# Kernel optimization log

Measured on AMD Instinct MI355X. Metric: run time of the kernel, lower is better.

Reference implementation:

```python
import jax, jax.numpy as jnp
import numpy as np

B, S, D = 8, 2048, 512

def setup_inputs() -> dict:
    key = jax.random.key(0)
    ks = jax.random.split(key, 9)
    scale = 1.0 / np.sqrt(D)
    q = jax.random.normal(ks[0], (B, S, D), dtype=jnp.float32)
    k = jax.random.normal(ks[1], (B, S, D), dtype=jnp.float32)
    v = jax.random.normal(ks[2], (B, S, D), dtype=jnp.float32)
    # causal mask, broadcast over batch: True = attend
    mask = jnp.tril(jnp.ones((S, S), dtype=bool))[None, :, :]
    Wq = jax.random.normal(ks[3], (D, D), dtype=jnp.float32) * scale
    bq = jax.random.normal(ks[4], (D,), dtype=jnp.float32) * scale
    Wk = jax.random.normal(ks[5], (D, D), dtype=jnp.float32) * scale
    bk = jax.random.normal(ks[6], (D,), dtype=jnp.float32) * scale
    Wv = jax.random.normal(ks[7], (D, D), dtype=jnp.float32) * scale
    bv = jax.random.normal(ks[8], (D,), dtype=jnp.float32) * scale
    return {"q": q, "k": k, "v": v, "mask": mask,
            "Wq": Wq, "bq": bq, "Wk": Wk, "bk": bk, "Wv": Wv, "bv": bv}

def reference(q, k, v, mask, Wq, bq, Wk, bk, Wv, bv):
    # torch nn.Linear: x @ W^T + b
    Q = jnp.einsum('bsd,ed->bse', q, Wq) + bq
    K = jnp.einsum('bsd,ed->bse', k, Wk) + bk
    V = jnp.einsum('bsd,ed->bse', v, Wv) + bv
    scores = jnp.einsum('bqd,bkd->bqk', Q, K) / jnp.sqrt(jnp.float32(D))
    scores = jnp.where(mask, scores, jnp.float32(-1e9))
    prob = jax.nn.softmax(scores, axis=-1)
    out = jnp.einsum('bqk,bkd->bqd', prob, V)
    return out
```

## Files before the change

### kernel.cpp

```cpp
#include <hip/hip_runtime.h>
#include <stdint.h>
#include <stddef.h>

typedef _Float16 half8 __attribute__((ext_vector_type(8)));
typedef float f32x4 __attribute__((ext_vector_type(4)));

#define SCALE_QK 0.04419417382415922f

__device__ __forceinline__ void gload16(const void* g, void* lds) {
  __builtin_amdgcn_global_load_lds(
      (const __attribute__((address_space(1))) void*)g,
      (__attribute__((address_space(3))) void*)lds,
      16, 0, 0);
}

template<bool A_F32>
__device__ __forceinline__ void run_kloop(const void* Arow0, const _Float16* Brow0,
                                          int lda, int ldb, int kIters,
                                          _Float16* As, _Float16* Bs,
                                          f32x4 (&acc)[4][4])
{
  const int tid  = threadIdx.x;
  const int lane = tid & 63;
  const int w    = tid >> 6;
  const int wm   = w >> 1, wn = w & 1;
  const int srow = tid >> 3;
  const int sg   = tid & 7;
  const int swz  = sg ^ (srow & 7);
  const int fr   = lane & 15;
  const int fq   = lane >> 4;
  const int fx   = lane & 7;

  for (int it = 0; it < kIters; ++it) {
    const int k0 = it * 64;
    __syncthreads();
    if constexpr (A_F32) {
      const float* A = (const float*)Arow0;
      #pragma unroll
      for (int i = 0; i < 4; ++i) {
        const float* src = A + (size_t)(i*32 + srow) * lda + (k0 + sg*8);
        f32x4 x = *(const f32x4*)src;
        f32x4 y = *(const f32x4*)(src + 4);
        half8 h;
        h[0]=(_Float16)x[0]; h[1]=(_Float16)x[1]; h[2]=(_Float16)x[2]; h[3]=(_Float16)x[3];
        h[4]=(_Float16)y[0]; h[5]=(_Float16)y[1]; h[6]=(_Float16)y[2]; h[7]=(_Float16)y[3];
        *(half8*)(As + (i*32 + srow)*64 + swz*8) = h;
      }
    } else {
      const _Float16* A = (const _Float16*)Arow0;
      #pragma unroll
      for (int i = 0; i < 4; ++i) {
        const _Float16* src = A + (size_t)(i*32 + srow) * lda + (k0 + swz*8);
        gload16(src, As + i*2048 + w*512);
      }
    }
    #pragma unroll
    for (int i = 0; i < 4; ++i) {
      const _Float16* src = Brow0 + (size_t)(i*32 + srow) * ldb + (k0 + swz*8);
      gload16(src, Bs + i*2048 + w*512);
    }
    __syncthreads();

    #pragma unroll
    for (int ks = 0; ks < 2; ++ks) {
      half8 av[4], bv[4];
      const int slot = (ks*4 + fq) ^ fx;
      #pragma unroll
      for (int i = 0; i < 4; ++i) {
        av[i] = *(const half8*)(As + (wm*64 + i*16 + fr)*64 + slot*8);
        bv[i] = *(const half8*)(Bs + (wn*64 + i*16 + fr)*64 + slot*8);
      }
      #pragma unroll
      for (int i = 0; i < 4; ++i) {
        #pragma unroll
        for (int j = 0; j < 4; ++j) {
          acc[i][j] = __builtin_amdgcn_mfma_f32_16x16x32_f16(av[i], bv[j], acc[i][j], 0, 0, 0);
        }
      }
    }
  }
}

__global__ __launch_bounds__(256) void k_cvtw(const float* __restrict__ Wq,
                                              const float* __restrict__ Wk,
                                              const float* __restrict__ Wv,
                                              _Float16* __restrict__ Wb)
{
  const int t = blockIdx.x * 256 + threadIdx.x;
  const int base = t * 8;
  const int z = base >> 18;
  const int off = base & 262143;
  const float* src = (z == 0) ? Wq : ((z == 1) ? Wk : Wv);
  f32x4 a = *(const f32x4*)(src + off);
  f32x4 b = *(const f32x4*)(src + off + 4);
  half8 h;
  h[0]=(_Float16)a[0]; h[1]=(_Float16)a[1]; h[2]=(_Float16)a[2]; h[3]=(_Float16)a[3];
  h[4]=(_Float16)b[0]; h[5]=(_Float16)b[1]; h[6]=(_Float16)b[2]; h[7]=(_Float16)b[3];
  *(half8*)(Wb + base) = h;
}

__global__ __launch_bounds__(256) void k_proj(const float* __restrict__ q,
                                              const float* __restrict__ k,
                                              const float* __restrict__ v,
                                              const _Float16* __restrict__ Wb,
                                              const float* __restrict__ bq,
                                              const float* __restrict__ bk,
                                              const float* __restrict__ bv,
                                              _Float16* __restrict__ Qb,
                                              _Float16* __restrict__ Kb,
                                              _Float16* __restrict__ Vb)
{
  __shared__ __align__(16) _Float16 As[128*64];
  __shared__ __align__(16) _Float16 Bs[128*64];
  const int z = blockIdx.z;
  const float* A     = (z == 0) ? q  : (z == 1) ? k  : v;
  const float* bia   = (z == 0) ? bq : (z == 1) ? bk : bv;
  const _Float16* B  = Wb + (size_t)z * 512 * 512;
  _Float16* C        = (z == 0) ? Qb : (z == 1) ? Kb : Vb;
  const int mt = blockIdx.y, nt = blockIdx.x;

  f32x4 acc[4][4] = {};
  run_kloop<true>(A + (size_t)mt*128*512, B + (size_t)nt*128*512, 512, 512, 8, As, Bs, acc);

  const int lane = threadIdx.x & 63, w = threadIdx.x >> 6;
  const int wm = w >> 1, wn = w & 1;
  const int fr = lane & 15, fq = lane >> 4;
  #pragma unroll
  for (int j = 0; j < 4; ++j) {
    const int col = nt*128 + wn*64 + j*16 + fr;
    const float bval = bia[col];
    #pragma unroll
    for (int i = 0; i < 4; ++i) {
      const int row = mt*128 + wm*64 + i*16 + fq*4;
      #pragma unroll
      for (int r = 0; r < 4; ++r)
        C[(size_t)(row + r) * 512 + col] = (_Float16)(acc[i][j][r] + bval);
    }
  }
}

__global__ __launch_bounds__(256) void k_trans(const _Float16* __restrict__ Vb,
                                               _Float16* __restrict__ Vt)
{
  __shared__ __align__(16) _Float16 t[64][72];
  const int st = blockIdx.x, dt = blockIdx.y, b = blockIdx.z;
  const int r = threadIdx.x >> 2, g = threadIdx.x & 3;
  const _Float16* src = Vb + ((size_t)b*2048 + st*64 + r)*512 + dt*64 + g*16;
  half8 v0 = *(const half8*)src;
  half8 v1 = *(const half8*)(src + 8);
  *(half8*)&t[r][g*16]     = v0;
  *(half8*)&t[r][g*16 + 8] = v1;
  __syncthreads();
  half8 o0, o1;
  #pragma unroll
  for (int i2 = 0; i2 < 8; ++i2) o0[i2] = t[g*16 + i2][r];
  #pragma unroll
  for (int i2 = 0; i2 < 8; ++i2) o1[i2] = t[g*16 + 8 + i2][r];
  _Float16* dst = Vt + ((size_t)b*512 + dt*64 + r)*2048 + st*64 + g*16;
  *(half8*)dst       = o0;
  *(half8*)(dst + 8) = o1;
}

__global__ __launch_bounds__(256) void k_scores(const _Float16* __restrict__ Qb,
                                                const _Float16* __restrict__ Kb,
                                                _Float16* __restrict__ P)
{
  const int kt = blockIdx.x, qt = blockIdx.y, b = blockIdx.z;
  if (kt > qt) return;
  __shared__ __align__(16) _Float16 As[128*64];
  __shared__ __align__(16) _Float16 Bs[128*64];
  f32x4 acc[4][4] = {};
  run_kloop<false>(Qb + ((size_t)b*2048 + qt*128)*512,
                   Kb + ((size_t)b*2048 + kt*128)*512,
                   512, 512, 8, As, Bs, acc);
  const int lane = threadIdx.x & 63, w = threadIdx.x >> 6;
  const int wm = w >> 1, wn = w & 1;
  const int fr = lane & 15, fq = lane >> 4;
  #pragma unroll
  for (int i = 0; i < 4; ++i) {
    const int row = qt*128 + wm*64 + i*16 + fq*4;
    #pragma unroll
    for (int j = 0; j < 4; ++j) {
      const int col = kt*128 + wn*64 + j*16 + fr;
      #pragma unroll
      for (int r = 0; r < 4; ++r)
        P[((size_t)b*2048 + row + r) * 2048 + col] = (_Float16)(acc[i][j][r] * SCALE_QK);
    }
  }
}

__global__ __launch_bounds__(256) void k_softmax(_Float16* __restrict__ P)
{
  const int lane = threadIdx.x & 63;
  const int row  = blockIdx.x * 4 + (threadIdx.x >> 6);
  const int qIdx = row & 2047;
  _Float16* p = P + (size_t)row * 2048;
  const int L    = qIdx + 1;
  const int Lpad = ((qIdx >> 7) + 1) * 128;

  float m = -1e30f;
  for (int i0 = lane * 8; i0 < L; i0 += 512) {
    if (i0 + 8 <= L) {
      half8 x = *(const half8*)(p + i0);
      #pragma unroll
      for (int j2 = 0; j2 < 8; ++j2) m = fmaxf(m, (float)x[j2]);
    } else {
      for (int j2 = 0; i0 + j2 < L; ++j2) m = fmaxf(m, (float)p[i0 + j2]);
    }
  }
  #pragma unroll
  for (int s = 1; s < 64; s <<= 1) m = fmaxf(m, __shfl_xor(m, s, 64));

  float lsum = 0.f;
  for (int i0 = lane * 8; i0 < L; i0 += 512) {
    if (i0 + 8 <= L) {
      half8 x = *(const half8*)(p + i0);
      #pragma unroll
      for (int j2 = 0; j2 < 8; ++j2) lsum += __expf((float)x[j2] - m);
    } else {
      for (int j2 = 0; i0 + j2 < L; ++j2) lsum += __expf((float)p[i0 + j2] - m);
    }
  }
  #pragma unroll
  for (int s = 1; s < 64; s <<= 1) lsum += __shfl_xor(lsum, s, 64);
  const float inv = 1.0f / lsum;

  for (int i0 = lane * 8; i0 < Lpad; i0 += 512) {
    half8 o;
    if (i0 + 8 <= L) {
      half8 x = *(const half8*)(p + i0);
      #pragma unroll
      for (int j2 = 0; j2 < 8; ++j2) o[j2] = (_Float16)(__expf((float)x[j2] - m) * inv);
    } else {
      #pragma unroll
      for (int j2 = 0; j2 < 8; ++j2) {
        const int idx = i0 + j2;
        o[j2] = (idx < L) ? (_Float16)(__expf((float)p[idx] - m) * inv) : (_Float16)0.f;
      }
    }
    *(half8*)(p + i0) = o;
  }
}

__global__ __launch_bounds__(256) void k_pv(const _Float16* __restrict__ P,
                                            const _Float16* __restrict__ Vt,
                                            float* __restrict__ Out)
{
  const int dt = blockIdx.x, b = blockIdx.z;
  const int yr = blockIdx.y;
  const int qt = (yr & 1) ? (15 - (yr >> 1)) : (yr >> 1);
  __shared__ __align__(16) _Float16 As[128*64];
  __shared__ __align__(16) _Float16 Bs[128*64];
  f32x4 acc[4][4] = {};
  run_kloop<false>(P  + ((size_t)b*2048 + qt*128)*2048,
                   Vt + ((size_t)b*512  + dt*128)*2048,
                   2048, 2048, (qt + 1) * 2, As, Bs, acc);
  const int lane = threadIdx.x & 63, w = threadIdx.x >> 6;
  const int wm = w >> 1, wn = w & 1;
  const int fr = lane & 15, fq = lane >> 4;
  #pragma unroll
  for (int i = 0; i < 4; ++i) {
    const int row = qt*128 + wm*64 + i*16 + fq*4;
    #pragma unroll
    for (int j = 0; j < 4; ++j) {
      const int col = dt*128 + wn*64 + j*16 + fr;
      #pragma unroll
      for (int r = 0; r < 4; ++r)
        Out[((size_t)b*2048 + row + r) * 512 + col] = acc[i][j][r];
    }
  }
}

extern "C" void kernel_launch(void* const* d_in, const int* in_sizes, int n_in,
                              void* d_out, int out_size, void* d_ws, size_t ws_size,
                              hipStream_t stream) {
  (void)in_sizes; (void)n_in; (void)out_size;
  const float* q  = (const float*)d_in[0];
  const float* k  = (const float*)d_in[1];
  const float* v  = (const float*)d_in[2];
  const float* Wq = (const float*)d_in[4];
  const float* bq = (const float*)d_in[5];
  const float* Wk = (const float*)d_in[6];
  const float* bk = (const float*)d_in[7];
  const float* Wv = (const float*)d_in[8];
  const float* bv = (const float*)d_in[9];

  const size_t OFF_P  = 0;
  const size_t OFF_Q  = (size_t)64 << 20;
  const size_t OFF_K  = (size_t)80 << 20;
  const size_t OFF_V  = (size_t)96 << 20;
  const size_t OFF_VT = (size_t)112 << 20;
  const size_t OFF_W  = (size_t)128 << 20;
  const size_t NEEDED = OFF_W + (size_t)3 * 512 * 512 * sizeof(_Float16);
  if (ws_size < NEEDED) return;

  char* ws = (char*)d_ws;
  _Float16* P  = (_Float16*)(ws + OFF_P);
  _Float16* Qb = (_Float16*)(ws + OFF_Q);
  _Float16* Kb = (_Float16*)(ws + OFF_K);
  _Float16* Vb = (_Float16*)(ws + OFF_V);
  _Float16* Vt = (_Float16*)(ws + OFF_VT);
  _Float16* Wb = (_Float16*)(ws + OFF_W);
  float* Out = (float*)d_out;

  k_cvtw   <<<dim3(384),       dim3(256), 0, stream>>>(Wq, Wk, Wv, Wb);
  k_proj   <<<dim3(4, 128, 3), dim3(256), 0, stream>>>(q, k, v, Wb, bq, bk, bv, Qb, Kb, Vb);
  k_trans  <<<dim3(32, 8, 8),  dim3(256), 0, stream>>>(Vb, Vt);
  k_scores <<<dim3(16, 16, 8), dim3(256), 0, stream>>>(Qb, Kb, P);
  k_softmax<<<dim3(4096),      dim3(256), 0, stream>>>(P);
  k_pv     <<<dim3(4, 16, 8),  dim3(256), 0, stream>>>(P, Vt, Out);
}
```

Baseline: 309.5 us.

## Double-buffer LDS in GEMM k-loop and use online softmax

```diff
diff --git a/kernel.cpp b/kernel.cpp
--- a/kernel.cpp
+++ b/kernel.cpp
@@ -17,7 +17,7 @@
 template<bool A_F32>
 __device__ __forceinline__ void run_kloop(const void* Arow0, const _Float16* Brow0,
                                           int lda, int ldb, int kIters,
-                                          _Float16* As, _Float16* Bs,
+                                          _Float16 (*As)[128*64], _Float16 (*Bs)[128*64],
                                           f32x4 (&acc)[4][4])
 {
   const int tid  = threadIdx.x;
@@ -31,53 +31,87 @@
   const int fq   = lane >> 4;
   const int fx   = lane & 7;
 
-  for (int it = 0; it < kIters; ++it) {
+  f32x4 pre0[8], pre1[8];
+
+  auto issueA32 = [&](int it, f32x4 (&dst)[8]) {
+    const float* A = (const float*)Arow0;
     const int k0 = it * 64;
-    __syncthreads();
-    if constexpr (A_F32) {
-      const float* A = (const float*)Arow0;
-      #pragma unroll
-      for (int i = 0; i < 4; ++i) {
-        const float* src = A + (size_t)(i*32 + srow) * lda + (k0 + sg*8);
-        f32x4 x = *(const f32x4*)src;
-        f32x4 y = *(const f32x4*)(src + 4);
-        half8 h;
-        h[0]=(_Float16)x[0]; h[1]=(_Float16)x[1]; h[2]=(_Float16)x[2]; h[3]=(_Float16)x[3];
-        h[4]=(_Float16)y[0]; h[5]=(_Float16)y[1]; h[6]=(_Float16)y[2]; h[7]=(_Float16)y[3];
-        *(half8*)(As + (i*32 + srow)*64 + swz*8) = h;
-      }
-    } else {
-      const _Float16* A = (const _Float16*)Arow0;
-      #pragma unroll
-      for (int i = 0; i < 4; ++i) {
-        const _Float16* src = A + (size_t)(i*32 + srow) * lda + (k0 + swz*8);
-        gload16(src, As + i*2048 + w*512);
-      }
-    }
     #pragma unroll
     for (int i = 0; i < 4; ++i) {
-      const _Float16* src = Brow0 + (size_t)(i*32 + srow) * ldb + (k0 + swz*8);
-      gload16(src, Bs + i*2048 + w*512);
-    }
-    __syncthreads();
-
+      const float* src = A + (size_t)(i*32 + srow) * lda + (k0 + sg*8);
+      dst[2*i]   = *(const f32x4*)src;
+      dst[2*i+1] = *(const f32x4*)(src + 4);
+    }
+  };
+  auto writeA32 = [&](const f32x4 (&src)[8], _Float16* dstAs) {
+    #pragma unroll
+    for (int i = 0; i < 4; ++i) {
+      f32x4 x = src[2*i], y = src[2*i+1];
+      half8 h;
+      h[0]=(_Float16)x[0]; h[1]=(_Float16)x[1]; h[2]=(_Float16)x[2]; h[3]=(_Float16)x[3];
+      h[4]=(_Float16)y[0]; h[5]=(_Float16)y[1]; h[6]=(_Float16)y[2]; h[7]=(_Float16)y[3];
+      *(half8*)(dstAs + (i*32 + srow)*64 + swz*8) = h;
+    }
+  };
+  auto gloadA16 = [&](int it, _Float16* dstAs) {
+    const _Float16* A = (const _Float16*)Arow0;
+    const int k0 = it * 64;
+    #pragma unroll
+    for (int i = 0; i < 4; ++i)
+      gload16(A + (size_t)(i*32 + srow) * lda + (k0 + swz*8), dstAs + i*2048 + w*512);
+  };
+  auto gloadB = [&](int it, _Float16* dstBs) {
+    const int k0 = it * 64;
+    #pragma unroll
+    for (int i = 0; i < 4; ++i)
+      gload16(Brow0 + (size_t)(i*32 + srow) * ldb + (k0 + swz*8), dstBs + i*2048 + w*512);
+  };
+  auto compute = [&](const _Float16* cAs, const _Float16* cBs) {
     #pragma unroll
     for (int ks = 0; ks < 2; ++ks) {
       half8 av[4], bv[4];
       const int slot = (ks*4 + fq) ^ fx;
       #pragma unroll
       for (int i = 0; i < 4; ++i) {
-        av[i] = *(const half8*)(As + (wm*64 + i*16 + fr)*64 + slot*8);
-        bv[i] = *(const half8*)(Bs + (wn*64 + i*16 + fr)*64 + slot*8);
+        av[i] = *(const half8*)(cAs + (wm*64 + i*16 + fr)*64 + slot*8);
+        bv[i] = *(const half8*)(cBs + (wn*64 + i*16 + fr)*64 + slot*8);
       }
       #pragma unroll
       for (int i = 0; i < 4; ++i) {
         #pragma unroll
-        for (int j = 0; j < 4; ++j) {
+        for (int j = 0; j < 4; ++j)
           acc[i][j] = __builtin_amdgcn_mfma_f32_16x16x32_f16(av[i], bv[j], acc[i][j], 0, 0, 0);
-        }
       }
     }
+  };
+  auto kstep = [&](int it, _Float16* curAs, _Float16* curBs,
+                   _Float16* nxtAs, _Float16* nxtBs,
+                   f32x4 (&pCons)[8], f32x4 (&pIss)[8]) {
+    const bool more = (it + 1) < kIters;
+    if (more) {
+      gloadB(it + 1, nxtBs);
+      if constexpr (!A_F32) gloadA16(it + 1, nxtAs);
+      else if (it + 2 < kIters) issueA32(it + 2, pIss);
+    }
+    compute(curAs, curBs);
+    if (more) { if constexpr (A_F32) writeA32(pCons, nxtAs); }
+    __syncthreads();
+  };
+
+  if constexpr (A_F32) {
+    issueA32(0, pre0);
+    gloadB(0, Bs[0]);
+    writeA32(pre0, As[0]);
+    if (kIters > 1) issueA32(1, pre1);
+  } else {
+    gloadA16(0, As[0]);
+    gloadB(0, Bs[0]);
+  }
+  __syncthreads();
+
+  for (int it = 0; it < kIters; it += 2) {
+    kstep(it,     As[0], Bs[0], As[1], Bs[1], pre1, pre0);
+    kstep(it + 1, As[1], Bs[1], As[0], Bs[0], pre0, pre1);
   }
 }
 
@@ -110,8 +144,8 @@
                                               _Float16* __restrict__ Kb,
                                               _Float16* __restrict__ Vb)
 {
-  __shared__ __align__(16) _Float16 As[128*64];
-  __shared__ __align__(16) _Float16 Bs[128*64];
+  __shared__ __align__(16) _Float16 As[2][128*64];
+  __shared__ __align__(16) _Float16 Bs[2][128*64];
   const int z = blockIdx.z;
   const float* A     = (z == 0) ? q  : (z == 1) ? k  : v;
   const float* bia   = (z == 0) ? bq : (z == 1) ? bk : bv;
@@ -167,8 +201,8 @@
 {
   const int kt = blockIdx.x, qt = blockIdx.y, b = blockIdx.z;
   if (kt > qt) return;
-  __shared__ __align__(16) _Float16 As[128*64];
-  __shared__ __align__(16) _Float16 Bs[128*64];
+  __shared__ __align__(16) _Float16 As[2][128*64];
+  __shared__ __align__(16) _Float16 Bs[2][128*64];
   f32x4 acc[4][4] = {};
   run_kloop<false>(Qb + ((size_t)b*2048 + qt*128)*512,
                    Kb + ((size_t)b*2048 + kt*128)*512,
@@ -198,44 +232,48 @@
   const int L    = qIdx + 1;
   const int Lpad = ((qIdx >> 7) + 1) * 128;
 
-  float m = -1e30f;
+  float m = -1e30f, s = 0.f;
   for (int i0 = lane * 8; i0 < L; i0 += 512) {
+    float xv[8];
     if (i0 + 8 <= L) {
       half8 x = *(const half8*)(p + i0);
       #pragma unroll
-      for (int j2 = 0; j2 < 8; ++j2) m = fmaxf(m, (float)x[j2]);
+      for (int j = 0; j < 8; ++j) xv[j] = (float)x[j];
     } else {
-      for (int j2 = 0; i0 + j2 < L; ++j2) m = fmaxf(m, (float)p[i0 + j2]);
-    }
-  }
-  #pragma unroll
-  for (int s = 1; s < 64; s <<= 1) m = fmaxf(m, __shfl_xor(m, s, 64));
-
-  float lsum = 0.f;
-  for (int i0 = lane * 8; i0 < L; i0 += 512) {
-    if (i0 + 8 <= L) {
-      half8 x = *(const half8*)(p + i0);
-      #pragma unroll
-      for (int j2 = 0; j2 < 8; ++j2) lsum += __expf((float)x[j2] - m);
-    } else {
-      for (int j2 = 0; i0 + j2 < L; ++j2) lsum += __expf((float)p[i0 + j2] - m);
-    }
-  }
-  #pragma unroll
-  for (int s = 1; s < 64; s <<= 1) lsum += __shfl_xor(lsum, s, 64);
-  const float inv = 1.0f / lsum;
+      #pragma unroll
+      for (int j = 0; j < 8; ++j) xv[j] = (i0 + j < L) ? (float)p[i0 + j] : -1e30f;
+    }
+    float cm = xv[0];
+    #pragma unroll
+    for (int j = 1; j < 8; ++j) cm = fmaxf(cm, xv[j]);
+    const float mn = fmaxf(m, cm);
+    float cs = 0.f;
+    #pragma unroll
+    for (int j = 0; j < 8; ++j) cs += __expf(xv[j] - mn);
+    s = s * __expf(m - mn) + cs;
+    m = mn;
+  }
+  #pragma unroll
+  for (int d = 1; d < 64; d <<= 1) {
+    const float mo = __shfl_xor(m, d, 64);
+    const float so = __shfl_xor(s, d, 64);
+    const float mn = fmaxf(m, mo);
+    s = s * __expf(m - mn) + so * __expf(mo - mn);
+    m = mn;
+  }
+  const float inv = 1.0f / s;
 
   for (int i0 = lane * 8; i0 < Lpad; i0 += 512) {
     half8 o;
     if (i0 + 8 <= L) {
       half8 x = *(const half8*)(p + i0);
       #pragma unroll
-      for (int j2 = 0; j2 < 8; ++j2) o[j2] = (_Float16)(__expf((float)x[j2] - m) * inv);
+      for (int j = 0; j < 8; ++j) o[j] = (_Float16)(__expf((float)x[j] - m) * inv);
     } else {
       #pragma unroll
-      for (int j2 = 0; j2 < 8; ++j2) {
-        const int idx = i0 + j2;
-        o[j2] = (idx < L) ? (_Float16)(__expf((float)p[idx] - m) * inv) : (_Float16)0.f;
+      for (int j = 0; j < 8; ++j) {
+        const int idx = i0 + j;
+        o[j] = (idx < L) ? (_Float16)(__expf((float)p[idx] - m) * inv) : (_Float16)0.f;
       }
     }
     *(half8*)(p + i0) = o;
@@ -249,8 +287,8 @@
   const int dt = blockIdx.x, b = blockIdx.z;
   const int yr = blockIdx.y;
   const int qt = (yr & 1) ? (15 - (yr >> 1)) : (yr >> 1);
-  __shared__ __align__(16) _Float16 As[128*64];
-  __shared__ __align__(16) _Float16 Bs[128*64];
+  __shared__ __align__(16) _Float16 As[2][128*64];
+  __shared__ __align__(16) _Float16 Bs[2][128*64];
   f32x4 acc[4][4] = {};
   run_kloop<false>(P  + ((size_t)b*2048 + qt*128)*2048,
                    Vt + ((size_t)b*512  + dt*128)*2048,
```

Result: slower. 326.4 us (+5.4%).
